# Kernel tuning notes

Measured on AMD Instinct MI355X. Metric: run time of the kernel, lower is better.

## Reference

```python
import jax, jax.numpy as jnp
import numpy as np

TAU = 2.0
V_TH = 1.0
V_RESET = 0.5

T, B, N = 64, 32, 32768


def setup_inputs() -> dict:
    key = jax.random.key(0)
    x = jax.random.normal(key, (T, B, N), dtype=jnp.float32)
    return {"x": x}


def reference(x):
    # Multi-step LIF, decay_input=False, hard reset to V_RESET.
    # H[t] = V[t-1] - (V[t-1] - V_RESET)/TAU + x[t]
    # S[t] = Heaviside(H[t] - V_TH)
    # V[t] = H[t]*(1-S[t]) + V_RESET*S[t]
    v0 = jnp.full(x.shape[1:], V_RESET, dtype=x.dtype)

    def step(v, xt):
        h = v - (v - V_RESET) / TAU + xt
        s = (h >= V_TH).astype(xt.dtype)
        v_new = h * (1.0 - s) + V_RESET * s
        return v_new, s

    _, spikes = jax.lax.scan(step, v0, x)
    return spikes  # (T, B, N)
```

## Files before the change

### kernel.cpp

```cpp
#include <hip/hip_runtime.h>


#define T_STEPS 64

__global__ __launch_bounds__(256) void lif_kernel(const float4* __restrict__ x,
                                                  float4* __restrict__ out,
                                                  int bn4) {
    int idx = blockIdx.x * blockDim.x + threadIdx.x;
    if (idx >= bn4) return;

    float4 v = make_float4(0.5f, 0.5f, 0.5f, 0.5f);

    #pragma unroll 4
    for (int t = 0; t < T_STEPS; ++t) {
        float4 xt = x[(size_t)t * bn4 + idx];
        float4 s;

        float hx = fmaf(0.5f, v.x, 0.25f + xt.x);
        float hy = fmaf(0.5f, v.y, 0.25f + xt.y);
        float hz = fmaf(0.5f, v.z, 0.25f + xt.z);
        float hw = fmaf(0.5f, v.w, 0.25f + xt.w);

        s.x = (hx >= 1.0f) ? 1.0f : 0.0f;
        s.y = (hy >= 1.0f) ? 1.0f : 0.0f;
        s.z = (hz >= 1.0f) ? 1.0f : 0.0f;
        s.w = (hw >= 1.0f) ? 1.0f : 0.0f;

        v.x = (hx >= 1.0f) ? 0.5f : hx;
        v.y = (hy >= 1.0f) ? 0.5f : hy;
        v.z = (hz >= 1.0f) ? 0.5f : hz;
        v.w = (hw >= 1.0f) ? 0.5f : hw;

        out[(size_t)t * bn4 + idx] = s;
    }
}

extern "C" void kernel_launch(void* const* d_in, const int* in_sizes, int n_in,
                              void* d_out, int out_size, void* d_ws, size_t ws_size,
                              hipStream_t stream) {
    const float4* x = (const float4*)d_in[0];
    float4* out = (float4*)d_out;

    int total = in_sizes[0];
    int bn = total / T_STEPS;
    int bn4 = bn / 4;

    int block = 256;
    int grid = (bn4 + block - 1) / block;
    lif_kernel<<<grid, block, 0, stream>>>(x, out, bn4);
}
```

Before: 119.9 us.

## Switch LIF kernel to float2 per thread with nontemporal loads and stores

Each thread now handles two neurons instead of four, which doubles the thread count to raise parallelism and memory-level concurrency. Loads and stores use nontemporal builtins so streaming data bypasses cache retention. The loop advances pointers incrementally, is unrolled 8 deep, and the launch bounds request higher occupancy. Narrower 8-byte accesses may use fewer bytes per memory instruction than the float4 version.

```diff
diff --git a/kernel.cpp b/kernel.cpp
--- a/kernel.cpp
+++ b/kernel.cpp
@@ -3,49 +3,51 @@
 
 #define T_STEPS 64
 
-__global__ __launch_bounds__(256) void lif_kernel(const float4* __restrict__ x,
-                                                  float4* __restrict__ out,
-                                                  int bn4) {
+typedef float f2 __attribute__((ext_vector_type(2)));
+
+__global__ __launch_bounds__(256, 8) void lif_kernel(const f2* __restrict__ x,
+                                                     f2* __restrict__ out,
+                                                     int bn2) {
     int idx = blockIdx.x * blockDim.x + threadIdx.x;
-    if (idx >= bn4) return;
+    if (idx >= bn2) return;
 
-    float4 v = make_float4(0.5f, 0.5f, 0.5f, 0.5f);
+    const f2* __restrict__ xp = x + idx;
+    f2* __restrict__ op = out + idx;
 
-    #pragma unroll 4
+    f2 v = {0.5f, 0.5f};
+
+    #pragma unroll 8
     for (int t = 0; t < T_STEPS; ++t) {
-        float4 xt = x[(size_t)t * bn4 + idx];
-        float4 s;
+        f2 xt = __builtin_nontemporal_load(xp);
+        f2 s;
 
         float hx = fmaf(0.5f, v.x, 0.25f + xt.x);
         float hy = fmaf(0.5f, v.y, 0.25f + xt.y);
-        float hz = fmaf(0.5f, v.z, 0.25f + xt.z);
-        float hw = fmaf(0.5f, v.w, 0.25f + xt.w);
 
         s.x = (hx >= 1.0f) ? 1.0f : 0.0f;
         s.y = (hy >= 1.0f) ? 1.0f : 0.0f;
-        s.z = (hz >= 1.0f) ? 1.0f : 0.0f;
-        s.w = (hw >= 1.0f) ? 1.0f : 0.0f;
 
         v.x = (hx >= 1.0f) ? 0.5f : hx;
         v.y = (hy >= 1.0f) ? 0.5f : hy;
-        v.z = (hz >= 1.0f) ? 0.5f : hz;
-        v.w = (hw >= 1.0f) ? 0.5f : hw;
 
-        out[(size_t)t * bn4 + idx] = s;
+        __builtin_nontemporal_store(s, op);
+
+        xp += bn2;
+        op += bn2;
     }
 }
 
 extern "C" void kernel_launch(void* const* d_in, const int* in_sizes, int n_in,
                               void* d_out, int out_size, void* d_ws, size_t ws_size,
                               hipStream_t stream) {
-    const float4* x = (const float4*)d_in[0];
-    float4* out = (float4*)d_out;
+    const f2* x = (const f2*)d_in[0];
+    f2* out = (f2*)d_out;
 
     int total = in_sizes[0];
     int bn = total / T_STEPS;
-    int bn4 = bn / 4;
+    int bn2 = bn / 2;
 
     int block = 256;
-    int grid = (bn4 + block - 1) / block;
-    lif_kernel<<<grid, block, 0, stream>>>(x, out, bn4);
+    int grid = (bn2 + block - 1) / block;
+    lif_kernel<<<grid, block, 0, stream>>>(x, out, bn2);
 }
```

Result: faster. 103.5 us (-13.7%).
